# Kernel optimization log

Measured on AMD Instinct MI355X. Metric: run time of the kernel, lower is better.

Reference implementation:

```python
import jax, jax.numpy as jnp
import numpy as np

B, T, C = 4, 2048, 1024
H, D = 16, 64
SCALE = D ** -0.5


def setup_inputs() -> dict:
    key = jax.random.key(0)
    ks = jax.random.split(key, 5)
    s = 0.02
    return {
        "hidden_states": jax.random.normal(ks[0], (B, T, C), dtype=jnp.float32),
        "attention_mask": jnp.ones((B, T), dtype=jnp.int32),
        "Wq": jax.random.normal(ks[1], (C, H * D), dtype=jnp.float32) * s,
        "Wk": jax.random.normal(ks[2], (C, H * D), dtype=jnp.float32) * s,
        "Wv": jax.random.normal(ks[3], (C, H * D), dtype=jnp.float32) * s,
        "Wo": jax.random.normal(ks[4], (H * D, C), dtype=jnp.float32) * s,
        "bo": jnp.zeros((C,), dtype=jnp.float32),
    }


def reference(hidden_states, attention_mask, Wq, Wk, Wv, Wo, bo):
    b, t, _ = hidden_states.shape
    # projections -> (B, H, T, D)
    q = (hidden_states @ Wq).reshape(b, t, H, D).transpose(0, 2, 1, 3)
    k = (hidden_states @ Wk).reshape(b, t, H, D).transpose(0, 2, 1, 3)
    v = (hidden_states @ Wv).reshape(b, t, H, D).transpose(0, 2, 1, 3)
    # scores (B, H, Tq, Tk)
    scores = jnp.einsum("bhqd,bhkd->bhqk", q, k) * SCALE
    mask = attention_mask[:, None, None, :]  # (B,1,1,T), dim==2 branch
    scores = jnp.where(mask == 0, -jnp.inf, scores)
    probs = jax.nn.softmax(scores, axis=-1)
    out = jnp.einsum("bhqk,bhkd->bhqd", probs, v)
    out = out.transpose(0, 2, 1, 3).reshape(b, t, H * D)
    return out @ Wo + bo
```

## Files before the change

kernel.cpp:

```cpp
#include <hip/hip_runtime.h>
#include <hip/hip_bf16.h>

#define B_ 4
#define T_ 2048
#define C_ 1024
#define H_ 16
#define D_ 64
#define SCALE_ 0.125f
#define L2E 1.4426950408889634f
#define SE (SCALE_ * L2E)

typedef __attribute__((ext_vector_type(8))) short bf16x8;
typedef __attribute__((ext_vector_type(4))) float f32x4;

__device__ __forceinline__ unsigned short f2bf(float f) {
    union { float f; unsigned u; } v; v.f = f;
    unsigned r = v.u + 0x7fff + ((v.u >> 16) & 1);
    return (unsigned short)(r >> 16);
}

__device__ __forceinline__ unsigned pk2bf(float a, float b) {
    __hip_bfloat162 t = __float22bfloat162_rn(make_float2(a, b));
    union { __hip_bfloat162 h; unsigned u; } c; c.h = t;
    return c.u;
}

__device__ __forceinline__ void gl_lds16(const unsigned short* g, unsigned short* l) {
    __builtin_amdgcn_global_load_lds(
        (const __attribute__((address_space(1))) void*)g,
        (__attribute__((address_space(3))) void*)l,
        16, 0, 0);
}

__device__ __forceinline__ void bar_fence() {
    asm volatile("s_barrier" ::: "memory");
}

__global__ void cvtw_kernel(const float4* __restrict__ in, ushort4* __restrict__ out,
                            const float* __restrict__ Wq, const float* __restrict__ Wk,
                            const float* __restrict__ Wv, const float* __restrict__ Wo,
                            unsigned short* __restrict__ Wqkv_t, unsigned short* __restrict__ Wo_t) {
    __shared__ float tile[64][65];
    const int bid = blockIdx.x;
    const int t = threadIdx.x;
    if (bid < 8192) {
        int i = bid * 256 + t;
        float4 v = in[i];
        ushort4 o;
        o.x = f2bf(v.x); o.y = f2bf(v.y); o.z = f2bf(v.z); o.w = f2bf(v.w);
        out[i] = o;
        return;
    }
    const int wb = bid - 8192;
    const int mtx = wb >> 8;
    const float* W = (mtx == 0) ? Wq : (mtx == 1) ? Wk : (mtx == 2) ? Wv : Wo;
    unsigned short* Out = (mtx < 3) ? (Wqkv_t + (size_t)mtx * 1024 * 1024) : Wo_t;
    const int tl = wb & 255;
    const int tx = tl & 15, ty = tl >> 4;
    const int col = t & 63, rb = t >> 6;
#pragma unroll
    for (int rr = 0; rr < 16; ++rr) {
        int r = rb * 16 + rr;
        tile[r][col] = W[(size_t)(ty * 64 + r) * 1024 + tx * 64 + col];
    }
    __syncthreads();
#pragma unroll
    for (int rr = 0; rr < 16; ++rr) {
        int r = rb * 16 + rr;
        Out[(size_t)(tx * 64 + r) * 1024 + ty * 64 + col] = f2bf(tile[col][r]);
    }
}

__device__ __forceinline__ void qkv_stage_A(
    const unsigned short* __restrict__ A, unsigned short* Lsh,
    int slot, int kt, int m0, int tid, int w) {
#pragma unroll
    for (int i = 0; i < 2; ++i) {
        int idx = i * 512 + tid;
        int r = idx >> 3;
        int c2 = ((idx & 7) * 16) ^ ((r & 7) << 4);
        gl_lds16(A + (size_t)(m0 + r) * 1024 + kt * 64 + (c2 >> 1),
                 Lsh + slot * 8192 + (i * 512 + w * 64) * 8);
    }
}

__device__ __forceinline__ void qkv_stage_B(
    const unsigned short* __restrict__ Bt, unsigned short* Lsh,
    int slot, int kt, int n0, int tid, int w) {
#pragma unroll
    for (int i = 0; i < 4; ++i) {
        int idx = i * 512 + tid;
        int r = idx >> 3;
        int c2 = ((idx & 7) * 16) ^ ((r & 7) << 4);
        gl_lds16(Bt + (size_t)(n0 + r) * 1024 + kt * 64 + (c2 >> 1),
                 Lsh + 16384 + slot * 16384 + (i * 512 + w * 64) * 8);
    }
}

__device__ __forceinline__ void gemm_128x256_loop(
    const unsigned short* __restrict__ A, const unsigned short* __restrict__ Bt,
    unsigned short* Lsh, f32x4 (&acc)[4][4],
    int m0, int n0, int tid, int w, int wr, int wc, int quad, int l16) {
    qkv_stage_A(A, Lsh, 0, 0, m0, tid, w);
    qkv_stage_B(Bt, Lsh, 0, 0, n0, tid, w);
    asm volatile("s_waitcnt vmcnt(0)" ::: "memory");
    bar_fence();

#pragma unroll 1
    for (int kt = 0; kt < 16; ++kt) {
        const int slot = kt & 1;
        qkv_stage_A(A, Lsh, slot ^ 1, (kt + 1) & 15, m0, tid, w);
        qkv_stage_B(Bt, Lsh, slot ^ 1, (kt + 1) & 15, n0, tid, w);

#pragma unroll
        for (int ks = 0; ks < 2; ++ks) {
            bf16x8 a[4], b[4];
#pragma unroll
            for (int i = 0; i < 4; ++i) {
                int r = wr * 64 + i * 16 + l16;
                int cb = (ks * 64 + quad * 16) ^ ((r & 7) << 4);
                a[i] = *(const bf16x8*)(Lsh + slot * 8192 + r * 64 + (cb >> 1));
            }
#pragma unroll
            for (int j = 0; j < 4; ++j) {
                int r = wc * 64 + j * 16 + l16;
                int cb = (ks * 64 + quad * 16) ^ ((r & 7) << 4);
                b[j] = *(const bf16x8*)(Lsh + 16384 + slot * 16384 + r * 64 + (cb >> 1));
            }
            __builtin_amdgcn_s_setprio(1);
#pragma unroll
            for (int i = 0; i < 4; ++i)
#pragma unroll
                for (int j = 0; j < 4; ++j)
                    acc[i][j] = __builtin_amdgcn_mfma_f32_16x16x32_bf16(a[i], b[j], acc[i][j], 0, 0, 0);
            __builtin_amdgcn_s_setprio(0);
        }
        asm volatile("s_waitcnt vmcnt(0)" ::: "memory");
        bar_fence();
    }
}

__global__ __launch_bounds__(512, 2) void gemm_qkv_kernel(
    const unsigned short* __restrict__ A, const unsigned short* __restrict__ Bt,
    unsigned short* __restrict__ Qg, unsigned short* __restrict__ Kf, unsigned short* __restrict__ Vf) {
    __shared__ __align__(16) unsigned short Lsh[49152];

    const int tid = threadIdx.x;
    const int w = tid >> 6, lane = tid & 63;
    const int quad = lane >> 4, l16 = lane & 15;
    const int wr = w >> 2, wc = w & 3;
    const int bid = blockIdx.x;
    const int swz = (bid & 7) * 96 + (bid >> 3);
    const int m0 = (swz & 63) * 128, n0 = (swz >> 6) * 256;

    const f32x4 fzero = {0.f, 0.f, 0.f, 0.f};
    f32x4 acc[4][4];
#pragma unroll
    for (int i = 0; i < 4; ++i)
#pragma unroll
        for (int j = 0; j < 4; ++j) acc[i][j] = fzero;

    gemm_128x256_loop(A, Bt, Lsh, acc, m0, n0, tid, w, wr, wc, quad, l16);

#pragma unroll
    for (int j = 0; j < 4; ++j) {
        int gn = n0 + wc * 64 + j * 16 + l16;
        int tensor = gn >> 10;
        int nl = gn & 1023;
        int hh = nl >> 6, dd = nl & 63;
#pragma unroll
        for (int i = 0; i < 4; ++i) {
            int gmb = m0 + wr * 64 + i * 16 + quad * 4;
            int bb = gmb >> 11;
            size_t bhh = (size_t)(bb * 16 + hh);
            if (tensor == 0) {
#pragma unroll
                for (int r = 0; r < 4; ++r) {
                    int tt = (gmb + r) & 2047;
                    Qg[(bhh * 2048 + tt) * 64 + dd] = f2bf(acc[i][j][r] * SE);
                }
            } else if (tensor == 1) {
#pragma unroll
                for (int r = 0; r < 4; ++r) {
                    int tt = (gmb + r) & 2047;
                    Kf[bhh * 131072 + (size_t)(tt >> 4) * 1024 + (dd >> 5) * 512 +
                       (((dd >> 3) & 3) * 16 + (tt & 15)) * 8 + (dd & 7)] = f2bf(acc[i][j][r]);
                }
            } else {
                int tt = gmb & 2047;
                ushort4 v4;
                v4.x = f2bf(acc[i][j][0]); v4.y = f2bf(acc[i][j][1]);
                v4.z = f2bf(acc[i][j][2]); v4.w = f2bf(acc[i][j][3]);
                *(ushort4*)(Vf + bhh * 131072 + (size_t)(tt >> 5) * 2048 + (dd >> 4) * 512 +
                            (((tt >> 3) & 3) * 16 + (dd & 15)) * 8 + (tt & 7)) = v4;
            }
        }
    }
}

__global__ __launch_bounds__(512, 2) void gemm_out_kernel(
    const unsigned short* __restrict__ A, const unsigned short* __restrict__ Bt,
    const float* __restrict__ bo, float* __restrict__ out) {
    __shared__ __align__(16) unsigned short Lsh[49152];

    const int tid = threadIdx.x;
    const int w = tid >> 6, lane = tid & 63;
    const int quad = lane >> 4, l16 = lane & 15;
    const int wr = w >> 2, wc = w & 3;
    const int bid = blockIdx.x;
    const int swz = (bid & 7) * 32 + (bid >> 3);
    const int m0 = (swz & 63) * 128, n0 = (swz >> 6) * 256;

    const f32x4 fzero = {0.f, 0.f, 0.f, 0.f};
    f32x4 acc[4][4];
#pragma unroll
    for (int i = 0; i < 4; ++i)
#pragma unroll
        for (int j = 0; j < 4; ++j) acc[i][j] = fzero;

    gemm_128x256_loop(A, Bt, Lsh, acc, m0, n0, tid, w, wr, wc, quad, l16);

#pragma unroll
    for (int j = 0; j < 4; ++j) {
        int gn = n0 + wc * 64 + j * 16 + l16;
        float bias = bo[gn];
#pragma unroll
        for (int i = 0; i < 4; ++i) {
            int gmb = m0 + wr * 64 + i * 16 + quad * 4;
#pragma unroll
            for (int r = 0; r < 4; ++r)
                out[(size_t)(gmb + r) * 1024 + gn] = acc[i][j][r] + bias;
        }
    }
}

template <bool CHECK_MASK>
__device__ __forceinline__ void attn_step_staged(
    int k0, const unsigned short* Kc, const unsigned short* Vc,
    unsigned short* Kn, unsigned short* Vn, int kn0,
    const unsigned short* __restrict__ Kg, const unsigned short* __restrict__ Vg,
    unsigned short* Pw, const bf16x8 (&aq)[2][2], const bf16x8& vones,
    f32x4 (&po)[2][4], f32x4 (&pl)[2],
    const int* __restrict__ mrow, int w, int lane, int quad, int l16) {

    gl_lds16(Kg + (size_t)(kn0 >> 4) * 1024 + w * 512 + lane * 8, Kn + w * 512);
    gl_lds16(Vg + (size_t)(kn0 >> 5) * 2048 + w * 512 + lane * 8, Vn + w * 512);

    bf16x8 ka0[4], ka1[4];
#pragma unroll
    for (int kt = 0; kt < 4; ++kt) {
        ka0[kt] = *(const bf16x8*)(Kc + kt * 1024 + lane * 8);
        ka1[kt] = *(const bf16x8*)(Kc + kt * 1024 + 512 + lane * 8);
    }

    const f32x4 fzero = {0.f, 0.f, 0.f, 0.f};
    bool allok = true;
    if (CHECK_MASK) {
        int mk = mrow[k0 + lane];
        allok = (__ballot(mk != 0) == 0xFFFFFFFFFFFFFFFFull);
    }

    if (allok) {
#pragma unroll
        for (int kt = 0; kt < 4; ++kt) {
            int pidx = ((((kt & 1) << 1) | (quad >> 1)) * 16 + l16) * 8 + (quad & 1) * 4;
#pragma unroll
            for (int qi = 0; qi < 2; ++qi) {
                f32x4 st = __builtin_amdgcn_mfma_f32_16x16x32_bf16(ka0[kt], aq[qi][0], fzero, 0, 0, 0);
                st = __builtin_amdgcn_mfma_f32_16x16x32_bf16(ka1[kt], aq[qi][1], st, 0, 0, 0);
                float p0 = __builtin_amdgcn_exp2f(st[0]);
                float p1 = __builtin_amdgcn_exp2f(st[1]);
                float p2 = __builtin_amdgcn_exp2f(st[2]);
                float p3 = __builtin_amdgcn_exp2f(st[3]);
                uint2 pk; pk.x = pk2bf(p0, p1); pk.y = pk2bf(p2, p3);
                *(uint2*)(Pw + (qi * 2 + (kt >> 1)) * 512 + pidx) = pk;
            }
        }
    } else {
#pragma unroll
        for (int kt = 0; kt < 4; ++kt) {
            int4 mv = *(const int4*)(mrow + k0 + kt * 16 + quad * 4);
            float mb0 = mv.x ? 0.f : -1e30f;
            float mb1 = mv.y ? 0.f : -1e30f;
            float mb2 = mv.z ? 0.f : -1e30f;
            float mb3 = mv.w ? 0.f : -1e30f;
            int pidx = ((((kt & 1) << 1) | (quad >> 1)) * 16 + l16) * 8 + (quad & 1) * 4;
#pragma unroll
            for (int qi = 0; qi < 2; ++qi) {
                f32x4 st = __builtin_amdgcn_mfma_f32_16x16x32_bf16(ka0[kt], aq[qi][0], fzero, 0, 0, 0);
                st = __builtin_amdgcn_mfma_f32_16x16x32_bf16(ka1[kt], aq[qi][1], st, 0, 0, 0);
                float p0 = __builtin_amdgcn_exp2f(st[0] + mb0);
                float p1 = __builtin_amdgcn_exp2f(st[1] + mb1);
                float p2 = __builtin_amdgcn_exp2f(st[2] + mb2);
                float p3 = __builtin_amdgcn_exp2f(st[3] + mb3);
                uint2 pk; pk.x = pk2bf(p0, p1); pk.y = pk2bf(p2, p3);
                *(uint2*)(Pw + (qi * 2 + (kt >> 1)) * 512 + pidx) = pk;
            }
        }
    }

    bf16x8 bv[2][4];
#pragma unroll
    for (int c = 0; c < 2; ++c)
#pragma unroll
        for (int nd = 0; nd < 4; ++nd)
            bv[c][nd] = *(const bf16x8*)(Vc + c * 2048 + nd * 512 + lane * 8);

    asm volatile("s_waitcnt lgkmcnt(0)" ::: "memory");

#pragma unroll
    for (int c = 0; c < 2; ++c)
#pragma unroll
        for (int qi = 0; qi < 2; ++qi) {
            bf16x8 ap = *(const bf16x8*)(Pw + (qi * 2 + c) * 512 + lane * 8);
#pragma unroll
            for (int nd = 0; nd < 4; ++nd)
                po[qi][nd] = __builtin_amdgcn_mfma_f32_16x16x32_bf16(ap, bv[c][nd], po[qi][nd], 0, 0, 0);
            pl[qi] = __builtin_amdgcn_mfma_f32_16x16x32_bf16(ap, vones, pl[qi], 0, 0, 0);
        }
}

__global__ __launch_bounds__(512, 4) void attn_kernel(
    const unsigned short* __restrict__ Qg, const unsigned short* __restrict__ Kf,
    const unsigned short* __restrict__ Vf, const int* __restrict__ mask,
    unsigned short* __restrict__ AO) {
    __shared__ __align__(16) unsigned short KsA[4096], KsB[4096];
    __shared__ __align__(16) unsigned short VsA[4096], VsB[4096];
    __shared__ __align__(16) unsigned short Pbuf[8][2048];

    const int tid = threadIdx.x;
    const int w = tid >> 6, lane = tid & 63;
    const int quad = lane >> 4, l16 = lane & 15;
    const int bid = blockIdx.x;
    const int bh = (bid & 7) * 8 + ((bid >> 6) & 7);
    const int qt = (bid >> 3) & 7;
    const int b = bh >> 4, h = bh & 15;
    const size_t bh_td = (size_t)bh * (2048 * 64);
    const int q0w = qt * 256 + w * 32;

    bf16x8 aq[2][2];
#pragma unroll
    for (int qi = 0; qi < 2; ++qi)
#pragma unroll
        for (int hh = 0; hh < 2; ++hh)
            aq[qi][hh] = *(const bf16x8*)(Qg + bh_td + (size_t)(q0w + qi * 16 + l16) * 64 + hh * 32 + quad * 8);

    const unsigned short* Kg = Kf + bh_td;
    const unsigned short* Vg = Vf + bh_td;
    const int* mrow = mask + b * 2048;

    bf16x8 vones;
#pragma unroll
    for (int i = 0; i < 8; ++i) vones[i] = (short)0x3F80;

    const f32x4 fzero = {0.f, 0.f, 0.f, 0.f};
    f32x4 po[2][4];
    f32x4 pl[2];
#pragma unroll
    for (int qi = 0; qi < 2; ++qi) {
        pl[qi] = fzero;
#pragma unroll
        for (int nd = 0; nd < 4; ++nd) po[qi][nd] = fzero;
    }

    bool okl = true;
#pragma unroll
    for (int r = 0; r < 8; ++r) {
        int4 m4 = *(const int4*)(mrow + r * 256 + lane * 4);
        okl = okl && (m4.x != 0) && (m4.y != 0) && (m4.z != 0) && (m4.w != 0);
    }
    const bool all_ok = (__ballot(okl) == 0xFFFFFFFFFFFFFFFFull);

    gl_lds16(Kg + w * 512 + lane * 8, KsA + w * 512);
    gl_lds16(Vg + w * 512 + lane * 8, VsA + w * 512);
    asm volatile("s_waitcnt vmcnt(0)" ::: "memory");
    __syncthreads();

    if (all_ok) {
#pragma unroll 1
        for (int k0 = 0; k0 < 2048; k0 += 128) {
            attn_step_staged<false>(k0, KsA, VsA, KsB, VsB, k0 + 64,
                                    Kg, Vg, Pbuf[w], aq, vones, po, pl, mrow, w, lane, quad, l16);
            asm volatile("s_waitcnt vmcnt(0)" ::: "memory");
            __syncthreads();
            attn_step_staged<false>(k0 + 64, KsB, VsB, KsA, VsA, (k0 + 128) & 2047,
                                    Kg, Vg, Pbuf[w], aq, vones, po, pl, mrow, w, lane, quad, l16);
            asm volatile("s_waitcnt vmcnt(0)" ::: "memory");
            __syncthreads();
        }
    } else {
#pragma unroll 1
        for (int k0 = 0; k0 < 2048; k0 += 128) {
            attn_step_staged<true>(k0, KsA, VsA, KsB, VsB, k0 + 64,
                                   Kg, Vg, Pbuf[w], aq, vones, po, pl, mrow, w, lane, quad, l16);
            asm volatile("s_waitcnt vmcnt(0)" ::: "memory");
            __syncthreads();
            attn_step_staged<true>(k0 + 64, KsB, VsB, KsA, VsA, (k0 + 128) & 2047,
                                   Kg, Vg, Pbuf[w], aq, vones, po, pl, mrow, w, lane, quad, l16);
            asm volatile("s_waitcnt vmcnt(0)" ::: "memory");
            __syncthreads();
        }
    }

#pragma unroll
    for (int qi = 0; qi < 2; ++qi)
#pragma unroll
        for (int r = 0; r < 4; ++r) {
            float linv = __builtin_amdgcn_rcpf(pl[qi][r]);
            int q = q0w + qi * 16 + quad * 4 + r;
            size_t ob = (size_t)(b * 2048 + q) * 1024 + h * 64;
#pragma unroll
            for (int nd = 0; nd < 4; ++nd)
                AO[ob + nd * 16 + l16] = f2bf(po[qi][nd][r] * linv);
        }
}

extern "C" void kernel_launch(void* const* d_in, const int* in_sizes, int n_in,
                              void* d_out, int out_size, void* d_ws, size_t ws_size,
                              hipStream_t stream) {
    const float* hs  = (const float*)d_in[0];
    const int* mask  = (const int*)d_in[1];
    const float* Wq  = (const float*)d_in[2];
    const float* Wk  = (const float*)d_in[3];
    const float* Wv  = (const float*)d_in[4];
    const float* Wo  = (const float*)d_in[5];
    const float* bo  = (const float*)d_in[6];
    float* out = (float*)d_out;

    char* ws = (char*)d_ws;
    unsigned short* hs_bf = (unsigned short*)(ws);
    unsigned short* wqkv  = (unsigned short*)(ws + 16777216);
    unsigned short* wo_t  = (unsigned short*)(ws + 23068672);
    unsigned short* Qg    = (unsigned short*)(ws + 25165824);
    unsigned short* Kf    = (unsigned short*)(ws + 41943040);
    unsigned short* Vf    = (unsigned short*)(ws + 58720256);
    unsigned short* AO    = (unsigned short*)(ws + 75497472);

    cvtw_kernel<<<9216, 256, 0, stream>>>((const float4*)hs, (ushort4*)hs_bf,
                                          Wq, Wk, Wv, Wo, wqkv, wo_t);
    gemm_qkv_kernel<<<768, 512, 0, stream>>>(hs_bf, wqkv, Qg, Kf, Vf);
    attn_kernel<<<512, 512, 0, stream>>>(Qg, Kf, Vf, mask, AO);
    gemm_out_kernel<<<256, 512, 0, stream>>>(AO, wo_t, bo, out);
}
```

Baseline: 272.4 us.

## Double per-wave query rows in attention to reuse K/V tiles across more queries

Each wave now processes 64 query rows instead of 32, so each block covers 512 queries and the grid halves to 256 blocks. Each K/V tile staged in LDS and loaded into registers is reused across twice as many query rows, cutting global and LDS K/V traffic per query. In exchange, the accumulator and Q register footprint doubles, the P buffer in LDS doubles, and launch bounds drop to 2 blocks per CU, which reduces occupancy. With 256 blocks there may also be fewer blocks than the hardware can run at once.

```diff
diff --git a/kernel.cpp b/kernel.cpp
--- a/kernel.cpp
+++ b/kernel.cpp
@@ -239,8 +239,9 @@
     int k0, const unsigned short* Kc, const unsigned short* Vc,
     unsigned short* Kn, unsigned short* Vn, int kn0,
     const unsigned short* __restrict__ Kg, const unsigned short* __restrict__ Vg,
-    unsigned short* Pw, const bf16x8 (&aq)[2][2], const bf16x8& vones,
-    f32x4 (&po)[2][4], f32x4 (&pl)[2],
+    unsigned short* Pw,
+    const bf16x8 (&aq)[2][2][2], const bf16x8& vones,
+    f32x4 (&po)[2][2][4], f32x4 (&pl)[2][2],
     const int* __restrict__ mrow, int w, int lane, int quad, int l16) {
 
     gl_lds16(Kg + (size_t)(kn0 >> 4) * 1024 + w * 512 + lane * 8, Kn + w * 512);
@@ -265,16 +266,18 @@
         for (int kt = 0; kt < 4; ++kt) {
             int pidx = ((((kt & 1) << 1) | (quad >> 1)) * 16 + l16) * 8 + (quad & 1) * 4;
 #pragma unroll
-            for (int qi = 0; qi < 2; ++qi) {
-                f32x4 st = __builtin_amdgcn_mfma_f32_16x16x32_bf16(ka0[kt], aq[qi][0], fzero, 0, 0, 0);
-                st = __builtin_amdgcn_mfma_f32_16x16x32_bf16(ka1[kt], aq[qi][1], st, 0, 0, 0);
-                float p0 = __builtin_amdgcn_exp2f(st[0]);
-                float p1 = __builtin_amdgcn_exp2f(st[1]);
-                float p2 = __builtin_amdgcn_exp2f(st[2]);
-                float p3 = __builtin_amdgcn_exp2f(st[3]);
-                uint2 pk; pk.x = pk2bf(p0, p1); pk.y = pk2bf(p2, p3);
-                *(uint2*)(Pw + (qi * 2 + (kt >> 1)) * 512 + pidx) = pk;
-            }
+            for (int s = 0; s < 2; ++s)
+#pragma unroll
+                for (int qi = 0; qi < 2; ++qi) {
+                    f32x4 st = __builtin_amdgcn_mfma_f32_16x16x32_bf16(ka0[kt], aq[s][qi][0], fzero, 0, 0, 0);
+                    st = __builtin_amdgcn_mfma_f32_16x16x32_bf16(ka1[kt], aq[s][qi][1], st, 0, 0, 0);
+                    float p0 = __builtin_amdgcn_exp2f(st[0]);
+                    float p1 = __builtin_amdgcn_exp2f(st[1]);
+                    float p2 = __builtin_amdgcn_exp2f(st[2]);
+                    float p3 = __builtin_amdgcn_exp2f(st[3]);
+                    uint2 pk; pk.x = pk2bf(p0, p1); pk.y = pk2bf(p2, p3);
+                    *(uint2*)(Pw + s * 2048 + (qi * 2 + (kt >> 1)) * 512 + pidx) = pk;
+                }
         }
     } else {
 #pragma unroll
@@ -286,16 +289,18 @@
             float mb3 = mv.w ? 0.f : -1e30f;
             int pidx = ((((kt & 1) << 1) | (quad >> 1)) * 16 + l16) * 8 + (quad & 1) * 4;
 #pragma unroll
-            for (int qi = 0; qi < 2; ++qi) {
-                f32x4 st = __builtin_amdgcn_mfma_f32_16x16x32_bf16(ka0[kt], aq[qi][0], fzero, 0, 0, 0);
-                st = __builtin_amdgcn_mfma_f32_16x16x32_bf16(ka1[kt], aq[qi][1], st, 0, 0, 0);
-                float p0 = __builtin_amdgcn_exp2f(st[0] + mb0);
-                float p1 = __builtin_amdgcn_exp2f(st[1] + mb1);
-                float p2 = __builtin_amdgcn_exp2f(st[2] + mb2);
-                float p3 = __builtin_amdgcn_exp2f(st[3] + mb3);
-                uint2 pk; pk.x = pk2bf(p0, p1); pk.y = pk2bf(p2, p3);
-                *(uint2*)(Pw + (qi * 2 + (kt >> 1)) * 512 + pidx) = pk;
-            }
+            for (int s = 0; s < 2; ++s)
+#pragma unroll
+                for (int qi = 0; qi < 2; ++qi) {
+                    f32x4 st = __builtin_amdgcn_mfma_f32_16x16x32_bf16(ka0[kt], aq[s][qi][0], fzero, 0, 0, 0);
+                    st = __builtin_amdgcn_mfma_f32_16x16x32_bf16(ka1[kt], aq[s][qi][1], st, 0, 0, 0);
+                    float p0 = __builtin_amdgcn_exp2f(st[0] + mb0);
+                    float p1 = __builtin_amdgcn_exp2f(st[1] + mb1);
+                    float p2 = __builtin_amdgcn_exp2f(st[2] + mb2);
+                    float p3 = __builtin_amdgcn_exp2f(st[3] + mb3);
+                    uint2 pk; pk.x = pk2bf(p0, p1); pk.y = pk2bf(p2, p3);
+                    *(uint2*)(Pw + s * 2048 + (qi * 2 + (kt >> 1)) * 512 + pidx) = pk;
+                }
         }
     }
 
@@ -309,41 +314,46 @@
     asm volatile("s_waitcnt lgkmcnt(0)" ::: "memory");
 
 #pragma unroll
-    for (int c = 0; c < 2; ++c)
-#pragma unroll
-        for (int qi = 0; qi < 2; ++qi) {
-            bf16x8 ap = *(const bf16x8*)(Pw + (qi * 2 + c) * 512 + lane * 8);
-#pragma unroll
-            for (int nd = 0; nd < 4; ++nd)
-                po[qi][nd] = __builtin_amdgcn_mfma_f32_16x16x32_bf16(ap, bv[c][nd], po[qi][nd], 0, 0, 0);
-            pl[qi] = __builtin_amdgcn_mfma_f32_16x16x32_bf16(ap, vones, pl[qi], 0, 0, 0);
-        }
-}
-
-__global__ __launch_bounds__(512, 4) void attn_kernel(
+    for (int s = 0; s < 2; ++s)
+#pragma unroll
+        for (int c = 0; c < 2; ++c)
+#pragma unroll
+            for (int qi = 0; qi < 2; ++qi) {
+                bf16x8 ap = *(const bf16x8*)(Pw + s * 2048 + (qi * 2 + c) * 512 + lane * 8);
+#pragma unroll
+                for (int nd = 0; nd < 4; ++nd)
+                    po[s][qi][nd] = __builtin_amdgcn_mfma_f32_16x16x32_bf16(ap, bv[c][nd], po[s][qi][nd], 0, 0, 0);
+                pl[s][qi] = __builtin_amdgcn_mfma_f32_16x16x32_bf16(ap, vones, pl[s][qi], 0, 0, 0);
+            }
+}
+
+__global__ __launch_bounds__(512, 2) void attn_kernel(
     const unsigned short* __restrict__ Qg, const unsigned short* __restrict__ Kf,
     const unsigned short* __restrict__ Vf, const int* __restrict__ mask,
     unsigned short* __restrict__ AO) {
     __shared__ __align__(16) unsigned short KsA[4096], KsB[4096];
     __shared__ __align__(16) unsigned short VsA[4096], VsB[4096];
-    __shared__ __align__(16) unsigned short Pbuf[8][2048];
+    __shared__ __align__(16) unsigned short Pbuf[8][4096];
 
     const int tid = threadIdx.x;
     const int w = tid >> 6, lane = tid & 63;
     const int quad = lane >> 4, l16 = lane & 15;
     const int bid = blockIdx.x;
-    const int bh = (bid & 7) * 8 + ((bid >> 6) & 7);
-    const int qt = (bid >> 3) & 7;
+    const int bh = (bid & 7) * 8 + ((bid >> 5) & 7);
+    const int qt = (bid >> 3) & 3;
     const int b = bh >> 4, h = bh & 15;
     const size_t bh_td = (size_t)bh * (2048 * 64);
-    const int q0w = qt * 256 + w * 32;
-
-    bf16x8 aq[2][2];
-#pragma unroll
-    for (int qi = 0; qi < 2; ++qi)
-#pragma unroll
-        for (int hh = 0; hh < 2; ++hh)
-            aq[qi][hh] = *(const bf16x8*)(Qg + bh_td + (size_t)(q0w + qi * 16 + l16) * 64 + hh * 32 + quad * 8);
+    const int q0w = qt * 512 + w * 64;
+
+    bf16x8 aq[2][2][2];
+#pragma unroll
+    for (int s = 0; s < 2; ++s)
+#pragma unroll
+        for (int qi = 0; qi < 2; ++qi)
+#pragma unroll
+            for (int hh = 0; hh < 2; ++hh)
+                aq[s][qi][hh] = *(const bf16x8*)(Qg + bh_td +
+                    (size_t)(q0w + (s * 2 + qi) * 16 + l16) * 64 + hh * 32 + quad * 8);
 
     const unsigned short* Kg = Kf + bh_td;
     const unsigned short* Vg = Vf + bh_td;
@@ -354,14 +364,16 @@
     for (int i = 0; i < 8; ++i) vones[i] = (short)0x3F80;
 
     const f32x4 fzero = {0.f, 0.f, 0.f, 0.f};
-    f32x4 po[2][4];
-    f32x4 pl[2];
-#pragma unroll
-    for (int qi = 0; qi < 2; ++qi) {
-        pl[qi] = fzero;
-#pragma unroll
-        for (int nd = 0; nd < 4; ++nd) po[qi][nd] = fzero;
-    }
+    f32x4 po[2][2][4];
+    f32x4 pl[2][2];
+#pragma unroll
+    for (int s = 0; s < 2; ++s)
+#pragma unroll
+        for (int qi = 0; qi < 2; ++qi) {
+            pl[s][qi] = fzero;
+#pragma unroll
+            for (int nd = 0; nd < 4; ++nd) po[s][qi][nd] = fzero;
+        }
 
     bool okl = true;
 #pragma unroll
@@ -403,16 +415,18 @@
     }
 
 #pragma unroll
-    for (int qi = 0; qi < 2; ++qi)
-#pragma unroll
-        for (int r = 0; r < 4; ++r) {
-            float linv = __builtin_amdgcn_rcpf(pl[qi][r]);
-            int q = q0w + qi * 16 + quad * 4 + r;
-            size_t ob = (size_t)(b * 2048 + q) * 1024 + h * 64;
-#pragma unroll
-            for (int nd = 0; nd < 4; ++nd)
-                AO[ob + nd * 16 + l16] = f2bf(po[qi][nd][r] * linv);
-        }
+    for (int s = 0; s < 2; ++s)
+#pragma unroll
+        for (int qi = 0; qi < 2; ++qi)
+#pragma unroll
+            for (int r = 0; r < 4; ++r) {
+                float linv = __builtin_amdgcn_rcpf(pl[s][qi][r]);
+                int q = q0w + (s * 2 + qi) * 16 + quad * 4 + r;
+                size_t ob = (size_t)(b * 2048 + q) * 1024 + h * 64;
+#pragma unroll
+                for (int nd = 0; nd < 4; ++nd)
+                    AO[ob + nd * 16 + l16] = f2bf(po[s][qi][nd][r] * linv);
+            }
 }
 
 extern "C" void kernel_launch(void* const* d_in, const int* in_sizes, int n_in,
@@ -439,6 +453,6 @@
     cvtw_kernel<<<9216, 256, 0, stream>>>((const float4*)hs, (ushort4*)hs_bf,
                                           Wq, Wk, Wv, Wo, wqkv, wo_t);
     gemm_qkv_kernel<<<768, 512, 0, stream>>>(hs_bf, wqkv, Qg, Kf, Vf);
-    attn_kernel<<<512, 512, 0, stream>>>(Qg, Kf, Vf, mask, AO);
+    attn_kernel<<<256, 512, 0, stream>>>(Qg, Kf, Vf, mask, AO);
     gemm_out_kernel<<<256, 512, 0, stream>>>(AO, wo_t, bo, out);
 }
```

New measurement: 272.7 us. About the same (+0.1%).

## Triple-buffer K/V tiles in LDS with deeper prefetch and one barrier per step

Applied to the files above, without the earlier changes.

Replaces the double-buffered K/V shared-memory staging with a three-slot ring buffer. The prefetch now runs two tiles ahead, and each step waits only for the older loads (vmcnt(2)) before one fence barrier, where before it drained all loads and synced twice. The aim is to hide global-to-LDS latency and cut barrier stalls. It costs 16KB more LDS per block, which may lower occupancy from the 4 blocks per CU requested in the launch bounds.

```diff
diff --git a/kernel.cpp b/kernel.cpp
--- a/kernel.cpp
+++ b/kernel.cpp
@@ -324,8 +324,8 @@
     const unsigned short* __restrict__ Qg, const unsigned short* __restrict__ Kf,
     const unsigned short* __restrict__ Vf, const int* __restrict__ mask,
     unsigned short* __restrict__ AO) {
-    __shared__ __align__(16) unsigned short KsA[4096], KsB[4096];
-    __shared__ __align__(16) unsigned short VsA[4096], VsB[4096];
+    __shared__ __align__(16) unsigned short Ks3[3 * 4096];
+    __shared__ __align__(16) unsigned short Vs3[3 * 4096];
     __shared__ __align__(16) unsigned short Pbuf[8][2048];
 
     const int tid = threadIdx.x;
@@ -371,34 +371,37 @@
     }
     const bool all_ok = (__ballot(okl) == 0xFFFFFFFFFFFFFFFFull);
 
-    gl_lds16(Kg + w * 512 + lane * 8, KsA + w * 512);
-    gl_lds16(Vg + w * 512 + lane * 8, VsA + w * 512);
-    asm volatile("s_waitcnt vmcnt(0)" ::: "memory");
-    __syncthreads();
-
+    gl_lds16(Kg + w * 512 + lane * 8, Ks3 + w * 512);
+    gl_lds16(Vg + w * 512 + lane * 8, Vs3 + w * 512);
+    gl_lds16(Kg + 4096 + w * 512 + lane * 8, Ks3 + 4096 + w * 512);
+    gl_lds16(Vg + 4096 + w * 512 + lane * 8, Vs3 + 4096 + w * 512);
+
+    int cbuf = 0;
     if (all_ok) {
 #pragma unroll 1
-        for (int k0 = 0; k0 < 2048; k0 += 128) {
-            attn_step_staged<false>(k0, KsA, VsA, KsB, VsB, k0 + 64,
-                                    Kg, Vg, Pbuf[w], aq, vones, po, pl, mrow, w, lane, quad, l16);
-            asm volatile("s_waitcnt vmcnt(0)" ::: "memory");
-            __syncthreads();
-            attn_step_staged<false>(k0 + 64, KsB, VsB, KsA, VsA, (k0 + 128) & 2047,
-                                    Kg, Vg, Pbuf[w], aq, vones, po, pl, mrow, w, lane, quad, l16);
-            asm volatile("s_waitcnt vmcnt(0)" ::: "memory");
-            __syncthreads();
+        for (int t = 0; t < 32; ++t) {
+            int sbuf = cbuf + 2; if (sbuf >= 3) sbuf -= 3;
+            asm volatile("s_waitcnt vmcnt(2)" ::: "memory");
+            bar_fence();
+            attn_step_staged<false>(t * 64, Ks3 + cbuf * 4096, Vs3 + cbuf * 4096,
+                                    Ks3 + sbuf * 4096, Vs3 + sbuf * 4096,
+                                    ((t + 2) * 64) & 2047,
+                                    Kg, Vg, Pbuf[w], aq, vones, po, pl,
+                                    mrow, w, lane, quad, l16);
+            cbuf = cbuf + 1; if (cbuf >= 3) cbuf = 0;
         }
     } else {
 #pragma unroll 1
-        for (int k0 = 0; k0 < 2048; k0 += 128) {
-            attn_step_staged<true>(k0, KsA, VsA, KsB, VsB, k0 + 64,
-                                   Kg, Vg, Pbuf[w], aq, vones, po, pl, mrow, w, lane, quad, l16);
-            asm volatile("s_waitcnt vmcnt(0)" ::: "memory");
-            __syncthreads();
-            attn_step_staged<true>(k0 + 64, KsB, VsB, KsA, VsA, (k0 + 128) & 2047,
-                                   Kg, Vg, Pbuf[w], aq, vones, po, pl, mrow, w, lane, quad, l16);
-            asm volatile("s_waitcnt vmcnt(0)" ::: "memory");
-            __syncthreads();
+        for (int t = 0; t < 32; ++t) {
+            int sbuf = cbuf + 2; if (sbuf >= 3) sbuf -= 3;
+            asm volatile("s_waitcnt vmcnt(2)" ::: "memory");
+            bar_fence();
+            attn_step_staged<true>(t * 64, Ks3 + cbuf * 4096, Vs3 + cbuf * 4096,
+                                   Ks3 + sbuf * 4096, Vs3 + sbuf * 4096,
+                                   ((t + 2) * 64) & 2047,
+                                   Kg, Vg, Pbuf[w], aq, vones, po, pl,
+                                   mrow, w, lane, quad, l16);
+            cbuf = cbuf + 1; if (cbuf >= 3) cbuf = 0;
         }
     }
 
```

Result: no change. 274.6 us (+0.8%).
